# Kernel optimization log

Measured on AMD Instinct MI355X. Metric: run time of the kernel, lower is better.

## Reference

```python
import jax, jax.numpy as jnp
import numpy as np

B, S, HIDDEN, H, KVH, D = 4, 1024, 4096, 32, 8, 128
ROT = D // 2  # rotary_dim = head_size/2 (inv_freq over arange(0, dim, 2))
NUM_SLOTS = 8192
ROPE_THETA = 10000.0


def setup_inputs() -> dict:
    key = jax.random.key(0)
    k0, k1, k2 = jax.random.split(key, 3)
    T = B * S
    hidden_states = jax.random.normal(k0, (T, HIDDEN), dtype=jnp.float32) * 0.02
    # RoPE tables: positions 0..S-1 per sequence, gathered per token, shape [T,1,ROT]
    inv_freq = 1.0 / (ROPE_THETA ** (np.arange(0, D, 2, dtype=np.float32) / D))
    pos = jnp.tile(jnp.arange(S, dtype=jnp.float32), B)          # [T]
    freqs = pos[:, None] * jnp.asarray(inv_freq)[None, :]        # [T, ROT]
    cos = jnp.cos(freqs)[:, None, :]
    sin = jnp.sin(freqs)[:, None, :]
    w_qkv = jax.random.normal(k1, (H * D + 2 * KVH * D, HIDDEN), dtype=jnp.float32) * 0.02
    w_o = jax.random.normal(k2, (HIDDEN, H * D), dtype=jnp.float32) * 0.02
    slots = jnp.arange(T, dtype=jnp.int32)
    key_cache = jnp.zeros((NUM_SLOTS, KVH, D), dtype=jnp.float32)
    value_cache = jnp.zeros((NUM_SLOTS, KVH, D), dtype=jnp.float32)
    return {"hidden_states": hidden_states, "cos": cos, "sin": sin,
            "w_qkv": w_qkv, "w_o": w_o,
            "key_cache": key_cache, "value_cache": value_cache,
            "slots": slots, "seq_len": S}


def _rope(x, cos, sin):
    # x: [T, heads, D]; cos/sin: [T, 1, ROT]; NeoX half-split rotation
    x1, x2 = x[..., :ROT], x[..., ROT:2 * ROT]
    return jnp.concatenate([x1 * cos - x2 * sin, x1 * sin + x2 * cos], axis=-1)


def reference(hidden_states, cos, sin, w_qkv, w_o, key_cache, value_cache, slots, seq_len):
    T, hidden = hidden_states.shape
    kvh = key_cache.shape[1]
    d = key_cache.shape[2]
    h = (w_qkv.shape[0] - 2 * kvh * d) // d
    b = T // seq_len
    groups = h // kvh
    scale = d ** -0.5

    # fused QKV projection
    qkv = hidden_states @ w_qkv.T                              # [T, (h+2*kvh)*d]
    q = qkv[:, : h * d].reshape(T, h, d)
    k = qkv[:, h * d: h * d + kvh * d].reshape(T, kvh, d)
    v = qkv[:, h * d + kvh * d:].reshape(T, kvh, d)

    # in-place RoPE on query and key
    q = _rope(q, cos, sin)
    k = _rope(k, cos, sin)

    # reshape_and_cache: scatter rotated K and V into slot-indexed cache
    new_key_cache = key_cache.at[slots].set(k)
    new_value_cache = value_cache.at[slots].set(v)

    # prefill varlen flash attention (equal-length sequences), causal, GQA
    qb = q.reshape(b, seq_len, h, d)
    kb = jnp.repeat(k.reshape(b, seq_len, kvh, d), groups, axis=2)  # [b,s,h,d]
    vb = jnp.repeat(v.reshape(b, seq_len, kvh, d), groups, axis=2)
    scores = jnp.einsum('bqhd,bkhd->bhqk', qb, kb) * scale
    causal = jnp.tril(jnp.ones((seq_len, seq_len), dtype=bool))
    scores = jnp.where(causal[None, None], scores, jnp.finfo(scores.dtype).min)
    attn = jax.nn.softmax(scores, axis=-1)
    out = jnp.einsum('bhqk,bkhd->bqhd', attn, vb).reshape(T, h * d)

    return out @ w_o.T, new_key_cache, new_value_cache
```

## Files before the change

### kernel.cpp

```cpp
#include <hip/hip_runtime.h>
#include <hip/hip_bf16.h>

#define B_    4
#define S_    1024
#define HID   4096
#define H_    32
#define KVH_  8
#define D_    128
#define T_    (B_ * S_)
#define QKVD  (H_ * D_ + 2 * KVH_ * D_)
#define NSLOT 8192

typedef __attribute__((ext_vector_type(8))) short short8;
typedef __attribute__((ext_vector_type(4))) float f32x4;

__device__ __forceinline__ unsigned short f2b(float f) {
  union { __hip_bfloat16 h; unsigned short u; } c;
  c.h = __float2bfloat16(f);
  return c.u;
}
__device__ __forceinline__ float b2f(unsigned short u) {
  union { unsigned int i; float f; } c;
  c.i = ((unsigned int)u) << 16;
  return c.f;
}

__device__ __forceinline__ void async16(const void* g, void* l) {
  __builtin_amdgcn_global_load_lds(
      (const __attribute__((address_space(1))) unsigned int*)g,
      (__attribute__((address_space(3))) unsigned int*)l,
      16, 0, 0);
}

__global__ void conv_bf16(const float* __restrict__ src,
                          unsigned short* __restrict__ dst, int n4) {
  int i = blockIdx.x * 256 + threadIdx.x;
  if (i >= n4) return;
  float4 v = reinterpret_cast<const float4*>(src)[i];
  ushort4 o;
  o.x = f2b(v.x); o.y = f2b(v.y); o.z = f2b(v.z); o.w = f2b(v.w);
  reinterpret_cast<ushort4*>(dst)[i] = o;
}

template <bool BF16OUT>
__global__ __launch_bounds__(256) void gemm_bt(
    const unsigned short* __restrict__ A, const unsigned short* __restrict__ Bm,
    void* __restrict__ Cv, int M, int N, int K) {
  __shared__ unsigned short As[128 * 32];
  __shared__ unsigned short Bs[128 * 32];
  const int tid  = threadIdx.x;
  const int lane = tid & 63;
  const int w    = tid >> 6;
  const int quad = lane >> 4;
  const int l16  = lane & 15;
  const int bm = blockIdx.y * 128;
  const int bn = blockIdx.x * 128;
  const int wm = (w >> 1) * 64;
  const int wn = (w & 1) * 64;

  const int srow = tid >> 2;
  const int scol = (((tid & 3) ^ ((tid >> 3) & 3)) * 8);
  const int qoff = (quad ^ ((l16 >> 1) & 3)) * 8;

  const unsigned short* gA0 = A + (size_t)(bm + srow) * K + scol;
  const unsigned short* gA1 = A + (size_t)(bm + 64 + srow) * K + scol;
  const unsigned short* gB0 = Bm + (size_t)(bn + srow) * K + scol;
  const unsigned short* gB1 = Bm + (size_t)(bn + 64 + srow) * K + scol;
  unsigned short* lA0 = As + tid * 8;
  unsigned short* lA1 = As + 2048 + tid * 8;
  unsigned short* lB0 = Bs + tid * 8;
  unsigned short* lB1 = Bs + 2048 + tid * 8;

  const unsigned short* pa[4];
  const unsigned short* pb[4];
#pragma unroll
  for (int i = 0; i < 4; i++) {
    pa[i] = As + (wm + i * 16 + l16) * 32 + qoff;
    pb[i] = Bs + (wn + i * 16 + l16) * 32 + qoff;
  }

  f32x4 acc[4][4];
#pragma unroll
  for (int i = 0; i < 4; i++)
#pragma unroll
    for (int j = 0; j < 4; j++)
#pragma unroll
      for (int r = 0; r < 4; r++) acc[i][j][r] = 0.f;

  for (int k0 = 0; k0 < K; k0 += 32) {
    async16(gA0, lA0);
    async16(gA1, lA1);
    async16(gB0, lB0);
    async16(gB1, lB1);
    gA0 += 32; gA1 += 32; gB0 += 32; gB1 += 32;
    __syncthreads();
    short8 a[4], b[4];
#pragma unroll
    for (int i = 0; i < 4; i++) a[i] = *(const short8*)pa[i];
#pragma unroll
    for (int j = 0; j < 4; j++) b[j] = *(const short8*)pb[j];
#pragma unroll
    for (int i = 0; i < 4; i++)
#pragma unroll
      for (int j = 0; j < 4; j++)
        acc[i][j] = __builtin_amdgcn_mfma_f32_16x16x32_bf16(a[i], b[j], acc[i][j], 0, 0, 0);
    __syncthreads();
  }
  const int crow0 = bm + wm + quad * 4;
  const int ccol0 = bn + wn + l16;
  if constexpr (BF16OUT) {
    unsigned short* C = (unsigned short*)Cv;
#pragma unroll
    for (int i = 0; i < 4; i++)
#pragma unroll
      for (int j = 0; j < 4; j++)
#pragma unroll
        for (int r = 0; r < 4; r++)
          C[(size_t)(crow0 + i * 16 + r) * N + ccol0 + j * 16] = f2b(acc[i][j][r]);
  } else {
    float* C = (float*)Cv;
#pragma unroll
    for (int i = 0; i < 4; i++)
#pragma unroll
      for (int j = 0; j < 4; j++)
#pragma unroll
        for (int r = 0; r < 4; r++)
          C[(size_t)(crow0 + i * 16 + r) * N + ccol0 + j * 16] = acc[i][j][r];
  }
}

__global__ void rope_scatter(
    const unsigned short* __restrict__ qkv, const float* __restrict__ cosb,
    const float* __restrict__ sinb, const int* __restrict__ slots,
    unsigned short* __restrict__ qb, unsigned short* __restrict__ kb,
    unsigned short* __restrict__ vb, float* __restrict__ kco,
    float* __restrict__ vco) {
  const float sl2 = 0.08838834764831843f * 1.4426950408889634f;
  const int t = blockIdx.x;
  const int tid = threadIdx.x;
  const int b = t >> 10, s = t & 1023;
  const unsigned short* row = qkv + (size_t)t * QKVD;
  const float* cs = cosb + (size_t)t * 64;
  const float* sn = sinb + (size_t)t * 64;
  const int slot = slots[t];
  for (int wk = tid; wk < H_ * 64; wk += 256) {
    int hh = wk >> 6, i = wk & 63;
    float x1 = b2f(row[hh * D_ + i]), x2 = b2f(row[hh * D_ + 64 + i]);
    float c = cs[i], sv = sn[i];
    size_t base = ((size_t)(b * H_ + hh) * S_ + s) * D_;
    qb[base + i]      = f2b((x1 * c - x2 * sv) * sl2);
    qb[base + 64 + i] = f2b((x1 * sv + x2 * c) * sl2);
  }
  for (int wk = tid; wk < KVH_ * 64; wk += 256) {
    int hh = wk >> 6, i = wk & 63;
    float x1 = b2f(row[H_ * D_ + hh * D_ + i]);
    float x2 = b2f(row[H_ * D_ + hh * D_ + 64 + i]);
    float c = cs[i], sv = sn[i];
    float o1 = x1 * c - x2 * sv, o2 = x1 * sv + x2 * c;
    size_t base = ((size_t)(b * KVH_ + hh) * S_ + s) * D_;
    kb[base + i] = f2b(o1);
    kb[base + 64 + i] = f2b(o2);
    size_t cb = ((size_t)slot * KVH_ + hh) * D_;
    kco[cb + i] = o1;
    kco[cb + 64 + i] = o2;
  }
  for (int wk = tid; wk < KVH_ * D_; wk += 256) {
    int hh = wk >> 7, i = wk & 127;
    unsigned short xv = row[H_ * D_ + KVH_ * D_ + hh * D_ + i];
    vb[((size_t)(b * KVH_ + hh) * S_ + s) * D_ + i] = xv;
    vco[((size_t)slot * KVH_ + hh) * D_ + i] = b2f(xv);
  }
}

__global__ void transpose_v(const unsigned short* __restrict__ vb,
                            unsigned short* __restrict__ vt) {
  __shared__ unsigned short tile[64][65];
  const int bid = blockIdx.x;
  const int dt = bid & 1, st = (bid >> 1) & 15, bk = bid >> 5;
  const int tid = threadIdx.x;
  const unsigned short* src = vb + ((size_t)bk * S_ + st * 64) * D_ + dt * 64;
#pragma unroll
  for (int k = 0; k < 16; k++) {
    int e = k * 256 + tid, r = e >> 6, c = e & 63;
    tile[r][c] = src[(size_t)r * D_ + c];
  }
  __syncthreads();
  unsigned short* dst = vt + ((size_t)bk * D_ + dt * 64) * S_ + st * 64;
#pragma unroll
  for (int k = 0; k < 16; k++) {
    int e = k * 256 + tid, r = e >> 6, c = e & 63;
    dst[(size_t)r * S_ + c] = tile[c][r];
  }
}

__global__ __launch_bounds__(256) void attn_fused(
    const unsigned short* __restrict__ qb, const unsigned short* __restrict__ kb,
    const unsigned short* __restrict__ vt, unsigned short* __restrict__ ob) {
  __shared__ unsigned short Ks[4 * 64 * 32];
  __shared__ unsigned short Vs[2 * 128 * 32];
  __shared__ unsigned short Ps[4][2 * 16 * 32];
  const int tid = threadIdx.x;
  const int lane = tid & 63, w = tid >> 6;
  const int quad = lane >> 4, l16 = lane & 15;
  const int bidx = blockIdx.x;
  const int qt = 15 - (bidx & 15);
  const int bh = bidx >> 4;
  const int h = bh & 31, b = bh >> 5;
  const int kvh = h >> 2;
  const int q0 = qt * 64;
  const unsigned short* qbase = qb + ((size_t)bh * S_ + q0) * D_;
  const unsigned short* kbase = kb + (size_t)(b * KVH_ + kvh) * S_ * D_;
  const unsigned short* vbase = vt + (size_t)(b * KVH_ + kvh) * D_ * S_;

  const int srow = tid >> 2;
  const int scol = (((tid & 3) ^ ((tid >> 3) & 3)) * 8);
  const int qoff = (quad ^ ((l16 >> 1) & 3)) * 8;

#pragma unroll
  for (int i = 0; i < 4; i++)
    async16(qbase + (size_t)srow * D_ + i * 32 + scol, (unsigned short*)Ks + i * 2048 + tid * 8);
  __syncthreads();
  short8 qf[4];
#pragma unroll
  for (int kc = 0; kc < 4; kc++)
    qf[kc] = *(const short8*)(Ks + (kc * 64 + w * 16 + l16) * 32 + qoff);

  short8 of;
  {
    unsigned short ov = (l16 == 0) ? (unsigned short)0x3F80 : (unsigned short)0;
#pragma unroll
    for (int j = 0; j < 8; j++) of[j] = (short)ov;
  }

  f32x4 oac[8];
  f32x4 osum;
#pragma unroll
  for (int n = 0; n < 8; n++)
#pragma unroll
    for (int r = 0; r < 4; r++) oac[n][r] = 0.f;
#pragma unroll
  for (int r = 0; r < 4; r++) osum[r] = 0.f;
  float m_run[4] = {-3.0e38f, -3.0e38f, -3.0e38f, -3.0e38f};

  unsigned short* psw = &Ps[w][0];
  const int qrow = q0 + w * 16 + quad * 4;

  for (int jt = 0; jt <= qt; jt++) {
    __syncthreads();
    const int j0 = jt * 64;
#pragma unroll
    for (int i = 0; i < 4; i++)
      async16(kbase + (size_t)(j0 + srow) * D_ + i * 32 + scol,
              (unsigned short*)Ks + i * 2048 + tid * 8);
#pragma unroll
    for (int i = 0; i < 4; i++) {
      int kc = i >> 1;
      int d = (i & 1) * 64 + srow;
      async16(vbase + (size_t)d * S_ + j0 + kc * 32 + scol,
              (unsigned short*)Vs + i * 2048 + tid * 8);
    }
    __syncthreads();

    f32x4 sac[4];
#pragma unroll
    for (int t = 0; t < 4; t++)
#pragma unroll
      for (int r = 0; r < 4; r++) sac[t][r] = 0.f;
#pragma unroll
    for (int t = 0; t < 4; t++)
#pragma unroll
      for (int kc = 0; kc < 4; kc++)
        sac[t] = __builtin_amdgcn_mfma_f32_16x16x32_bf16(
            qf[kc], *(const short8*)(Ks + (kc * 64 + t * 16 + l16) * 32 + qoff),
            sac[t], 0, 0, 0);

    if (jt == qt) {
#pragma unroll
      for (int t = 0; t < 4; t++) {
        const int kcol = j0 + t * 16 + l16;
#pragma unroll
        for (int r = 0; r < 4; r++)
          if (kcol > qrow + r) sac[t][r] = -3.0e38f;
      }
    }
    float mx[4];
#pragma unroll
    for (int r = 0; r < 4; r++)
      mx[r] = fmaxf(fmaxf(sac[0][r], sac[1][r]), fmaxf(sac[2][r], sac[3][r]));
#pragma unroll
    for (int off = 1; off < 16; off <<= 1)
#pragma unroll
      for (int r = 0; r < 4; r++) mx[r] = fmaxf(mx[r], __shfl_xor(mx[r], off));
    float alpha[4];
#pragma unroll
    for (int r = 0; r < 4; r++) {
      float mn = fmaxf(m_run[r], mx[r]);
      alpha[r] = exp2f(m_run[r] - mn);
      m_run[r] = mn;
    }
#pragma unroll
    for (int t = 0; t < 4; t++)
#pragma unroll
      for (int r = 0; r < 4; r++) {
        float p = exp2f(sac[t][r] - m_run[r]);
        int prow = quad * 4 + r;
        int chunk = (((t & 1) * 2 + (l16 >> 3)) ^ ((prow >> 1) & 3));
        psw[(t >> 1) * 512 + prow * 32 + chunk * 8 + (l16 & 7)] = f2b(p);
      }
#pragma unroll
    for (int r = 0; r < 4; r++) osum[r] *= alpha[r];
#pragma unroll
    for (int n = 0; n < 8; n++)
#pragma unroll
      for (int r = 0; r < 4; r++) oac[n][r] *= alpha[r];
#pragma unroll
    for (int kc = 0; kc < 2; kc++) {
      short8 pf = *(const short8*)(psw + kc * 512 + l16 * 32 + qoff);
      osum = __builtin_amdgcn_mfma_f32_16x16x32_bf16(pf, of, osum, 0, 0, 0);
#pragma unroll
      for (int n = 0; n < 8; n++)
        oac[n] = __builtin_amdgcn_mfma_f32_16x16x32_bf16(
            pf, *(const short8*)(Vs + (kc * 128 + n * 16 + l16) * 32 + qoff),
            oac[n], 0, 0, 0);
    }
  }

  float inv[4];
#pragma unroll
  for (int r = 0; r < 4; r++) {
    float l = __shfl(osum[r], lane & 48, 64);
    inv[r] = 1.0f / l;
  }
  const size_t trow = (size_t)(b * S_ + q0 + w * 16 + quad * 4);
#pragma unroll
  for (int n = 0; n < 8; n++)
#pragma unroll
    for (int r = 0; r < 4; r++)
      ob[(trow + r) * (size_t)(H_ * D_) + h * D_ + n * 16 + l16] =
          f2b(oac[n][r] * inv[r]);
}

extern "C" void kernel_launch(void* const* d_in, const int* in_sizes, int n_in,
                              void* d_out, int out_size, void* d_ws, size_t ws_size,
                              hipStream_t stream) {
  const float* hidden = (const float*)d_in[0];
  const float* cosb   = (const float*)d_in[1];
  const float* sinb   = (const float*)d_in[2];
  const float* wqkv   = (const float*)d_in[3];
  const float* wo     = (const float*)d_in[4];
  const float* kc_in  = (const float*)d_in[5];
  const float* vc_in  = (const float*)d_in[6];
  const int*   slots  = (const int*)d_in[7];

  float* out    = (float*)d_out;
  float* kc_out = out + (size_t)T_ * HID;
  float* vc_out = kc_out + (size_t)NSLOT * KVH_ * D_;

  char* ws = (char*)d_ws;
  unsigned short* hb    = (unsigned short*)ws; ws += (size_t)T_ * HID * 2;
  unsigned short* wqkvb = (unsigned short*)ws; ws += (size_t)QKVD * HID * 2;
  unsigned short* wob   = (unsigned short*)ws; ws += (size_t)HID * HID * 2;
  unsigned short* qkv   = (unsigned short*)ws; ws += (size_t)T_ * QKVD * 2;
  unsigned short* qb    = (unsigned short*)ws; ws += (size_t)T_ * H_ * D_ * 2;
  unsigned short* kb    = (unsigned short*)ws; ws += (size_t)T_ * KVH_ * D_ * 2;
  unsigned short* vb    = (unsigned short*)ws; ws += (size_t)T_ * KVH_ * D_ * 2;
  unsigned short* vt    = (unsigned short*)ws; ws += (size_t)T_ * KVH_ * D_ * 2;
  unsigned short* ob    = (unsigned short*)ws;

  const size_t cache_bytes = (size_t)NSLOT * KVH_ * D_ * 4;
  hipMemcpyAsync(kc_out, kc_in, cache_bytes, hipMemcpyDeviceToDevice, stream);
  hipMemcpyAsync(vc_out, vc_in, cache_bytes, hipMemcpyDeviceToDevice, stream);

  conv_bf16<<<(T_ * HID / 4) / 256, 256, 0, stream>>>(hidden, hb, T_ * HID / 4);
  conv_bf16<<<(QKVD * HID / 4) / 256, 256, 0, stream>>>(wqkv, wqkvb, QKVD * HID / 4);
  conv_bf16<<<(HID * HID / 4) / 256, 256, 0, stream>>>(wo, wob, HID * HID / 4);

  dim3 g1(QKVD / 128, T_ / 128);
  gemm_bt<true><<<g1, 256, 0, stream>>>(hb, wqkvb, qkv, T_, QKVD, HID);

  rope_scatter<<<T_, 256, 0, stream>>>(qkv, cosb, sinb, slots, qb, kb, vb, kc_out, vc_out);

  transpose_v<<<B_ * KVH_ * 16 * 2, 256, 0, stream>>>(vb, vt);

  attn_fused<<<B_ * H_ * (S_ / 64), 256, 0, stream>>>(qb, kb, vt, ob);

  dim3 g2(HID / 128, T_ / 128);
  gemm_bt<false><<<g2, 256, 0, stream>>>(ob, wob, out, T_, HID, HID);
}
```

Before: 985.9 us.

## Rewrite GEMM with 256x256 tiles, double-buffered LDS prefetch and MFMA priority

The bf16 GEMM moves from 128x128 tiles with 256 threads to 256x256 tiles with 512 threads, each wave computing a 128x64 sub-tile. It double-buffers LDS with K-step 64, issuing async global-to-LDS loads for the next stage while MFMAs run. It uses vmcnt waits instead of full syncthreads and raises wave priority around the MFMA bursts. This aims to raise arithmetic intensity and hide memory latency, at the cost of more LDS (128KB), more registers per thread, and fewer blocks for the grid (QKV GEMM gets 24x16 blocks).

```diff
diff --git a/kernel.cpp b/kernel.cpp
--- a/kernel.cpp
+++ b/kernel.cpp
@@ -14,6 +14,9 @@
 typedef __attribute__((ext_vector_type(8))) short short8;
 typedef __attribute__((ext_vector_type(4))) float f32x4;
 
+#define MFMA_B16(d, x, y) \
+  d = __builtin_amdgcn_mfma_f32_16x16x32_bf16(x, y, d, 0, 0, 0)
+
 __device__ __forceinline__ unsigned short f2b(float f) {
   union { __hip_bfloat16 h; unsigned short u; } c;
   c.h = __float2bfloat16(f);
@@ -43,89 +46,136 @@
 }
 
 template <bool BF16OUT>
-__global__ __launch_bounds__(256) void gemm_bt(
+__global__ __launch_bounds__(512, 2) void gemm_bt(
     const unsigned short* __restrict__ A, const unsigned short* __restrict__ Bm,
     void* __restrict__ Cv, int M, int N, int K) {
-  __shared__ unsigned short As[128 * 32];
-  __shared__ unsigned short Bs[128 * 32];
+  __shared__ unsigned short As[2 * 2 * 256 * 32];
+  __shared__ unsigned short Bs[2 * 2 * 256 * 32];
   const int tid  = threadIdx.x;
   const int lane = tid & 63;
   const int w    = tid >> 6;
   const int quad = lane >> 4;
   const int l16  = lane & 15;
-  const int bm = blockIdx.y * 128;
-  const int bn = blockIdx.x * 128;
-  const int wm = (w >> 1) * 64;
-  const int wn = (w & 1) * 64;
-
-  const int srow = tid >> 2;
-  const int scol = (((tid & 3) ^ ((tid >> 3) & 3)) * 8);
+  const int bm = blockIdx.y * 256;
+  const int bn = blockIdx.x * 256;
+  const int wm = (w >> 2) * 128;
+  const int wn = (w & 3) * 64;
+
+  const int r0 = tid >> 2;
+  const int c0 = ((tid & 3) ^ ((r0 >> 1) & 3)) * 8;
+  const unsigned short* Ag = A + (size_t)(bm + r0) * K + c0;
+  const unsigned short* Bg = Bm + (size_t)(bn + r0) * K + c0;
+  const size_t rstep = (size_t)128 * K;
+
   const int qoff = (quad ^ ((l16 >> 1) & 3)) * 8;
-
-  const unsigned short* gA0 = A + (size_t)(bm + srow) * K + scol;
-  const unsigned short* gA1 = A + (size_t)(bm + 64 + srow) * K + scol;
-  const unsigned short* gB0 = Bm + (size_t)(bn + srow) * K + scol;
-  const unsigned short* gB1 = Bm + (size_t)(bn + 64 + srow) * K + scol;
-  unsigned short* lA0 = As + tid * 8;
-  unsigned short* lA1 = As + 2048 + tid * 8;
-  unsigned short* lB0 = Bs + tid * 8;
-  unsigned short* lB1 = Bs + 2048 + tid * 8;
-
-  const unsigned short* pa[4];
-  const unsigned short* pb[4];
-#pragma unroll
-  for (int i = 0; i < 4; i++) {
-    pa[i] = As + (wm + i * 16 + l16) * 32 + qoff;
-    pb[i] = Bs + (wn + i * 16 + l16) * 32 + qoff;
-  }
-
-  f32x4 acc[4][4];
-#pragma unroll
-  for (int i = 0; i < 4; i++)
-#pragma unroll
-    for (int j = 0; j < 4; j++)
-#pragma unroll
-      for (int r = 0; r < 4; r++) acc[i][j][r] = 0.f;
-
-  for (int k0 = 0; k0 < K; k0 += 32) {
-    async16(gA0, lA0);
-    async16(gA1, lA1);
-    async16(gB0, lB0);
-    async16(gB1, lB1);
-    gA0 += 32; gA1 += 32; gB0 += 32; gB1 += 32;
-    __syncthreads();
-    short8 a[4], b[4];
-#pragma unroll
-    for (int i = 0; i < 4; i++) a[i] = *(const short8*)pa[i];
-#pragma unroll
-    for (int j = 0; j < 4; j++) b[j] = *(const short8*)pb[j];
-#pragma unroll
-    for (int i = 0; i < 4; i++)
-#pragma unroll
-      for (int j = 0; j < 4; j++)
-        acc[i][j] = __builtin_amdgcn_mfma_f32_16x16x32_bf16(a[i], b[j], acc[i][j], 0, 0, 0);
-    __syncthreads();
-  }
+  const int aro = (wm + l16) * 32 + qoff;
+  const int bro = (wn + l16) * 32 + qoff;
+
+  f32x4 acc[8][4];
+#pragma unroll
+  for (int f = 0; f < 8; f++)
+#pragma unroll
+    for (int c = 0; c < 4; c++)
+#pragma unroll
+      for (int r = 0; r < 4; r++) acc[f][c][r] = 0.f;
+
+  unsigned short* lA = As + tid * 8;
+  unsigned short* lB = Bs + tid * 8;
+
+  async16(Ag,              lA);
+  async16(Ag + rstep,      lA + 4096);
+  async16(Bg,              lB);
+  async16(Bg + rstep,      lB + 4096);
+  async16(Ag + 32,         lA + 8192);
+  async16(Ag + rstep + 32, lA + 8192 + 4096);
+  async16(Bg + 32,         lB + 8192);
+  async16(Bg + rstep + 32, lB + 8192 + 4096);
+
+  const int KT = K >> 6;
+  for (int kt = 0; kt < KT; ++kt) {
+    const int cur = (kt & 1) << 14;
+    const int nxt = cur ^ 16384;
+    const size_t knx = (size_t)((kt + 1 < KT) ? (kt + 1) : kt) << 6;
+    const unsigned short* Ac = As + cur;
+    const unsigned short* Bc = Bs + cur;
+    unsigned short* An = As + nxt + tid * 8;
+    unsigned short* Bn = Bs + nxt + tid * 8;
+    short8 a[8], b0, b1;
+
+    async16(Ag + knx,         An);
+    async16(Ag + knx + rstep, An + 4096);
+    asm volatile("s_waitcnt vmcnt(4)" ::: "memory");
+    __builtin_amdgcn_s_barrier();
+#pragma unroll
+    for (int f = 0; f < 8; f++) a[f] = *(const short8*)(Ac + f * 512 + aro);
+    b0 = *(const short8*)(Bc + bro);
+    b1 = *(const short8*)(Bc + 512 + bro);
+    __builtin_amdgcn_s_setprio(1);
+#pragma unroll
+    for (int f = 0; f < 8; f++) MFMA_B16(acc[f][0], a[f], b0);
+#pragma unroll
+    for (int f = 0; f < 8; f++) MFMA_B16(acc[f][1], a[f], b1);
+    __builtin_amdgcn_s_setprio(0);
+
+    async16(Bg + knx,         Bn);
+    async16(Bg + knx + rstep, Bn + 4096);
+    b0 = *(const short8*)(Bc + 1024 + bro);
+    b1 = *(const short8*)(Bc + 1536 + bro);
+    __builtin_amdgcn_s_setprio(1);
+#pragma unroll
+    for (int f = 0; f < 8; f++) MFMA_B16(acc[f][2], a[f], b0);
+#pragma unroll
+    for (int f = 0; f < 8; f++) MFMA_B16(acc[f][3], a[f], b1);
+    __builtin_amdgcn_s_setprio(0);
+
+    async16(Ag + knx + 32,         An + 8192);
+    async16(Ag + knx + 32 + rstep, An + 8192 + 4096);
+    asm volatile("s_waitcnt vmcnt(4)" ::: "memory");
+    __builtin_amdgcn_s_barrier();
+#pragma unroll
+    for (int f = 0; f < 8; f++) a[f] = *(const short8*)(Ac + 8192 + f * 512 + aro);
+    b0 = *(const short8*)(Bc + 8192 + bro);
+    b1 = *(const short8*)(Bc + 8192 + 512 + bro);
+    __builtin_amdgcn_s_setprio(1);
+#pragma unroll
+    for (int f = 0; f < 8; f++) MFMA_B16(acc[f][0], a[f], b0);
+#pragma unroll
+    for (int f = 0; f < 8; f++) MFMA_B16(acc[f][1], a[f], b1);
+    __builtin_amdgcn_s_setprio(0);
+
+    async16(Bg + knx + 32,         Bn + 8192);
+    async16(Bg + knx + 32 + rstep, Bn + 8192 + 4096);
+    b0 = *(const short8*)(Bc + 8192 + 1024 + bro);
+    b1 = *(const short8*)(Bc + 8192 + 1536 + bro);
+    __builtin_amdgcn_s_setprio(1);
+#pragma unroll
+    for (int f = 0; f < 8; f++) MFMA_B16(acc[f][2], a[f], b0);
+#pragma unroll
+    for (int f = 0; f < 8; f++) MFMA_B16(acc[f][3], a[f], b1);
+    __builtin_amdgcn_s_setprio(0);
+  }
+  asm volatile("s_waitcnt vmcnt(0)" ::: "memory");
+
   const int crow0 = bm + wm + quad * 4;
   const int ccol0 = bn + wn + l16;
   if constexpr (BF16OUT) {
     unsigned short* C = (unsigned short*)Cv;
 #pragma unroll
-    for (int i = 0; i < 4; i++)
-#pragma unroll
-      for (int j = 0; j < 4; j++)
+    for (int f = 0; f < 8; f++)
+#pragma unroll
+      for (int c = 0; c < 4; c++)
 #pragma unroll
         for (int r = 0; r < 4; r++)
-          C[(size_t)(crow0 + i * 16 + r) * N + ccol0 + j * 16] = f2b(acc[i][j][r]);
+          C[(size_t)(crow0 + f * 16 + r) * N + ccol0 + c * 16] = f2b(acc[f][c][r]);
   } else {
     float* C = (float*)Cv;
 #pragma unroll
-    for (int i = 0; i < 4; i++)
-#pragma unroll
-      for (int j = 0; j < 4; j++)
+    for (int f = 0; f < 8; f++)
+#pragma unroll
+      for (int c = 0; c < 4; c++)
 #pragma unroll
         for (int r = 0; r < 4; r++)
-          C[(size_t)(crow0 + i * 16 + r) * N + ccol0 + j * 16] = acc[i][j][r];
+          C[(size_t)(crow0 + f * 16 + r) * N + ccol0 + c * 16] = acc[f][c][r];
   }
 }
 
@@ -375,8 +425,8 @@
   conv_bf16<<<(QKVD * HID / 4) / 256, 256, 0, stream>>>(wqkv, wqkvb, QKVD * HID / 4);
   conv_bf16<<<(HID * HID / 4) / 256, 256, 0, stream>>>(wo, wob, HID * HID / 4);
 
-  dim3 g1(QKVD / 128, T_ / 128);
-  gemm_bt<true><<<g1, 256, 0, stream>>>(hb, wqkvb, qkv, T_, QKVD, HID);
+  dim3 g1(QKVD / 256, T_ / 256);
+  gemm_bt<true><<<g1, 512, 0, stream>>>(hb, wqkvb, qkv, T_, QKVD, HID);
 
   rope_scatter<<<T_, 256, 0, stream>>>(qkv, cosb, sinb, slots, qb, kb, vb, kc_out, vc_out);
 
@@ -384,6 +434,6 @@
 
   attn_fused<<<B_ * H_ * (S_ / 64), 256, 0, stream>>>(qb, kb, vt, ob);
 
-  dim3 g2(HID / 128, T_ / 128);
-  gemm_bt<false><<<g2, 256, 0, stream>>>(ob, wob, out, T_, HID, HID);
-}
+  dim3 g2(HID / 256, T_ / 256);
+  gemm_bt<false><<<g2, 512, 0, stream>>>(ob, wob, out, T_, HID, HID);
+}
```

New measurement: 973.1 us. About the same (-1.3%).
